# Optimization experiments

Hardware: AMD Instinct MI355X
Metric: run time of the kernel (lower is better)

Reference implementation:

```python
import jax, jax.numpy as jnp
import numpy as np

N = 50000  # num nodes
EPS = 1e-06


def setup_inputs() -> dict:
    key = jax.random.key(0)
    ks = jax.random.split(key, 7)
    E = 800000
    nfeat, nhid, nclass = 64, 128, 64
    x = jax.random.normal(ks[0], (N, nfeat), dtype=jnp.float32)
    src = jax.random.randint(ks[1], (E,), 0, N, dtype=jnp.int32)
    dst = jax.random.randint(ks[2], (E,), 0, N, dtype=jnp.int32)
    W1 = jax.random.normal(ks[3], (nfeat, nhid), dtype=jnp.float32) * (1.0 / np.sqrt(nfeat))
    b1 = jnp.zeros((nhid,), dtype=jnp.float32)
    W2 = jax.random.normal(ks[4], (nhid, nclass), dtype=jnp.float32) * (1.0 / np.sqrt(nhid))
    b2 = jnp.zeros((nclass,), dtype=jnp.float32)
    return {"x": x, "src": src, "dst": dst, "W1": W1, "b1": b1, "W2": W2, "b2": b2}


def _sage_conv(h, src, dst, W, b):
    # spmm(adj, h): sum of neighbor features per destination row
    num = jax.ops.segment_sum(h[src], dst, num_segments=N)  # [N, d]
    # spmm(adj, ones_like(h)): per-row degree broadcast over features
    deg = jax.ops.segment_sum(jnp.ones((src.shape[0],), dtype=h.dtype), dst, num_segments=N)
    neighbor_mean = num / (deg[:, None] + EPS)
    return neighbor_mean @ W + b


def reference(x, src, dst, W1, b1, W2, b2):
    h = jax.nn.relu(_sage_conv(x, src, dst, W1, b1))
    # dropout is identity in eval mode (training=False)
    h = _sage_conv(h, src, dst, W2, b2)
    return jax.nn.log_softmax(h, axis=1)
```

## Files before the change

kernel.cpp:

```cpp
#include <hip/hip_runtime.h>
#include <hip/hip_fp16.h>

#define N_NODES 50000
#define EPS 1e-6f
#define NPAD 50048
#define CAP 64

#define NBKT 512
#define NPB 98
#define NROWS (NBKT * NPB)
#define BCAP 2048
#define CHUNK_A 3072
#define XH8 (N_NODES * 64 / 8)


#define COMP(v, j) ((j) == 0 ? (v).x : (j) == 1 ? (v).y : (j) == 2 ? (v).z : (v).w)

__device__ __forceinline__ float4 h4_to_f4(uint2 u) {
  __half2 h0 = *reinterpret_cast<__half2*>(&u.x);
  __half2 h1 = *reinterpret_cast<__half2*>(&u.y);
  float2 f0 = __half22float2(h0);
  float2 f1 = __half22float2(h1);
  float4 r; r.x = f0.x; r.y = f0.y; r.z = f1.x; r.w = f1.y;
  return r;
}

__global__ __launch_bounds__(256) void bucketize_kernel(
    const int* __restrict__ src, const int* __restrict__ dst,
    int* __restrict__ bcur, int* __restrict__ packed,
    const float* __restrict__ x, __half* __restrict__ xh, int E) {
  __shared__ int lcnt[NBKT];
  __shared__ int lbase[NBKT];
  int t = threadIdx.x;

  for (int i = blockIdx.x * 256 + t; i < XH8; i += gridDim.x * 256) {
    float4 a = ((const float4*)x)[2 * i];
    float4 b = ((const float4*)x)[2 * i + 1];
    __half2 h0 = __floats2half2_rn(a.x, a.y);
    __half2 h1 = __floats2half2_rn(a.z, a.w);
    __half2 h2 = __floats2half2_rn(b.x, b.y);
    __half2 h3 = __floats2half2_rn(b.z, b.w);
    uint4 o;
    o.x = *(unsigned int*)&h0; o.y = *(unsigned int*)&h1;
    o.z = *(unsigned int*)&h2; o.w = *(unsigned int*)&h3;
    ((uint4*)xh)[i] = o;
  }

  lcnt[t] = 0; lcnt[t + 256] = 0;
  __syncthreads();
  int base = blockIdx.x * CHUNK_A;
  int end = base + CHUNK_A; if (end > E) end = E;
  for (int e = base + t; e < end; e += 256) atomicAdd(&lcnt[dst[e] / NPB], 1);
  __syncthreads();
  {
    int c0 = lcnt[t], c1 = lcnt[t + 256];
    lbase[t]       = c0 ? atomicAdd(&bcur[t], c0) : 0;
    lbase[t + 256] = c1 ? atomicAdd(&bcur[t + 256], c1) : 0;
    lcnt[t] = 0; lcnt[t + 256] = 0;
  }
  __syncthreads();
  for (int e = base + t; e < end; e += 256) {
    int d = dst[e];
    int b = d / NPB;
    int pos = lbase[b] + atomicAdd(&lcnt[b], 1);
    if (pos < BCAP)
      packed[(b << 11) + pos] = (src[e] << 8) | (d - b * NPB);
  }
}

__global__ __launch_bounds__(256) void rows_kernel(
    const int* __restrict__ bcur, const int* __restrict__ packed,
    int* __restrict__ cnt, int* __restrict__ ssrc) {
  __shared__ int lout[NPB * 64];
  __shared__ int lcnt[NPB];
  int t = threadIdx.x;
  int b = blockIdx.x;
  if (t < NPB) lcnt[t] = 0;
  __syncthreads();
  int count = bcur[b]; if (count > BCAP) count = BCAP;
  const int* pk = packed + (b << 11);
  for (int i = t; i < count; i += 256) {
    int p = pk[i];
    int dl = p & 0xff;
    int pos = atomicAdd(&lcnt[dl], 1);
    if (pos < CAP) lout[(dl << 6) + pos] = p >> 8;
  }
  __syncthreads();
  int4* d4 = (int4*)(ssrc + (size_t)b * (NPB * 64));
  const int4* s4 = (const int4*)lout;
  for (int i = t; i < NPB * 16; i += 256) d4[i] = s4[i];
  if (t < NPB) {
    int c = lcnt[t]; if (c > CAP) c = CAP;
    cnt[b * NPB + t] = c;
  }
}

#define QADD(V0, V1, V2, V3) do {                                         \
    acc.x += ((V0).x + (V1).x) + ((V2).x + (V3).x);                       \
    acc.y += ((V0).y + (V1).y) + ((V2).y + (V3).y);                       \
    acc.z += ((V0).z + (V1).z) + ((V2).z + (V3).z);                       \
    acc.w += ((V0).w + (V1).w) + ((V2).w + (V3).w);                       \
  } while (0)

#define ADD1(V) do {                                                      \
    acc.x += (V).x; acc.y += (V).y; acc.z += (V).z; acc.w += (V).w;       \
  } while (0)

#define GATHER_STEP_H(SRCPTR)                                             \
  {                                                                       \
    int rem = e - base; if (rem > 16) rem = 16;                           \
    int s[16];                                                            \
    _Pragma("unroll")                                                     \
    for (int j = 0; j < 16; j++) s[j] = ssrc[base + j];                   \
    _Pragma("unroll")                                                     \
    for (int j = 0; j < 16; j++) { if (j >= rem) s[j] = 0; }              \
    uint2 v[16];                                                          \
    _Pragma("unroll")                                                     \
    for (int j = 0; j < 16; j++)                                          \
      v[j] = ((const uint2*)((SRCPTR) + (size_t)s[j] * 64))[l16];         \
    int rq = rem >> 2, rr = rem & 3;                                      \
    _Pragma("unroll")                                                     \
    for (int q = 0; q < 4; q++) {                                         \
      if (q < rq) {                                                       \
        float4 f0 = h4_to_f4(v[4 * q]);                                   \
        float4 f1 = h4_to_f4(v[4 * q + 1]);                               \
        float4 f2 = h4_to_f4(v[4 * q + 2]);                               \
        float4 f3 = h4_to_f4(v[4 * q + 3]);                               \
        QADD(f0, f1, f2, f3);                                             \
      }                                                                   \
    }                                                                     \
    _Pragma("unroll")                                                     \
    for (int q = 0; q < 4; q++) {                                         \
      if (q == rq && rr > 0) {                                            \
        float4 f0 = h4_to_f4(v[4 * q]);                                   \
        ADD1(f0);                                                         \
        if (rr > 1) { float4 f1 = h4_to_f4(v[4 * q + 1]); ADD1(f1); }     \
        if (rr > 2) { float4 f2 = h4_to_f4(v[4 * q + 2]); ADD1(f2); }     \
      }                                                                   \
    }                                                                     \
  }

__global__ __launch_bounds__(256) void gather1_kernel(
    const __half* __restrict__ xh, const int* __restrict__ cnt,
    const int* __restrict__ ssrc, __half* __restrict__ mean1h) {
  int t = threadIdx.x;
  int lane = t & 63;
  int sub = lane >> 4;
  int l16 = lane & 15;
  int node = blockIdx.x * 16 + ((t >> 6) << 2) + sub;
  int b = node << 6;
  int e = b + cnt[node];
  float4 acc = {0.f, 0.f, 0.f, 0.f};
  for (int base = b; base < e; base += 16) {
    GATHER_STEP_H(xh)
  }
  float dinv = 1.0f / ((float)(e - b) + EPS);
  __half2 p0 = __floats2half2_rn(acc.x * dinv, acc.y * dinv);
  __half2 p1 = __floats2half2_rn(acc.z * dinv, acc.w * dinv);
  uint2 o;
  o.x = *(unsigned int*)&p0; o.y = *(unsigned int*)&p1;
  ((uint2*)(mean1h + (size_t)node * 64))[l16] = o;
}

__global__ __launch_bounds__(256, 3) void mlp_fused_kernel(
    const __half* __restrict__ mean1h, const float* __restrict__ W1,
    const float* __restrict__ b1, const float* __restrict__ W2,
    __half* __restrict__ gh) {
  __shared__ float sM[64][68];
  __shared__ float sH[64][132];
  int t = threadIdx.x;
  int row0 = blockIdx.x * 64;

  {
    const uint2* M2 = (const uint2*)(mean1h + (size_t)row0 * 64);
#pragma unroll
    for (int i = 0; i < 4; i++) {
      int idx = t + 256 * i;
      float4 f = h4_to_f4(M2[idx]);
      *(float4*)&sM[idx >> 4][(idx & 15) << 2] = f;
    }
  }
  __syncthreads();

  int tc = t & 15;
  int tr = t >> 4;

  {
    int c = tc << 3;
    int r = tr << 2;
    float acc[4][8];
    float4 bA = *(const float4*)(b1 + c);
    float4 bB = *(const float4*)(b1 + c + 4);
#pragma unroll
    for (int i = 0; i < 4; i++) {
      acc[i][0] = bA.x; acc[i][1] = bA.y; acc[i][2] = bA.z; acc[i][3] = bA.w;
      acc[i][4] = bB.x; acc[i][5] = bB.y; acc[i][6] = bB.z; acc[i][7] = bB.w;
    }
#pragma unroll 1
    for (int k = 0; k < 64; k += 4) {
      float4 a[4];
#pragma unroll
      for (int i = 0; i < 4; i++) a[i] = *(const float4*)&sM[r + i][k];
      float4 wA[4], wB[4];
#pragma unroll
      for (int j = 0; j < 4; j++) {
        const float* wrow = W1 + (size_t)(k + j) * 128 + c;
        wA[j] = *(const float4*)wrow;
        wB[j] = *(const float4*)(wrow + 4);
      }
#pragma unroll
      for (int j = 0; j < 4; j++) {
#pragma unroll
        for (int i = 0; i < 4; i++) {
          float av = COMP(a[i], j);
          acc[i][0] = fmaf(av, wA[j].x, acc[i][0]);
          acc[i][1] = fmaf(av, wA[j].y, acc[i][1]);
          acc[i][2] = fmaf(av, wA[j].z, acc[i][2]);
          acc[i][3] = fmaf(av, wA[j].w, acc[i][3]);
          acc[i][4] = fmaf(av, wB[j].x, acc[i][4]);
          acc[i][5] = fmaf(av, wB[j].y, acc[i][5]);
          acc[i][6] = fmaf(av, wB[j].z, acc[i][6]);
          acc[i][7] = fmaf(av, wB[j].w, acc[i][7]);
        }
      }
    }
#pragma unroll
    for (int i = 0; i < 4; i++) {
      float4 h0, h1v;
      h0.x = fmaxf(acc[i][0], 0.f); h0.y = fmaxf(acc[i][1], 0.f);
      h0.z = fmaxf(acc[i][2], 0.f); h0.w = fmaxf(acc[i][3], 0.f);
      h1v.x = fmaxf(acc[i][4], 0.f); h1v.y = fmaxf(acc[i][5], 0.f);
      h1v.z = fmaxf(acc[i][6], 0.f); h1v.w = fmaxf(acc[i][7], 0.f);
      *(float4*)&sH[r + i][c] = h0;
      *(float4*)&sH[r + i][c + 4] = h1v;
    }
  }
  __syncthreads();

  {
    int c = tc << 2;
    int r = tr << 2;
    float acc[4][4];
#pragma unroll
    for (int i = 0; i < 4; i++)
      acc[i][0] = acc[i][1] = acc[i][2] = acc[i][3] = 0.f;
#pragma unroll 1
    for (int k = 0; k < 128; k += 4) {
      float4 a[4];
#pragma unroll
      for (int i = 0; i < 4; i++) a[i] = *(const float4*)&sH[r + i][k];
      float4 w[4];
#pragma unroll
      for (int j = 0; j < 4; j++)
        w[j] = *(const float4*)(W2 + (size_t)(k + j) * 64 + c);
#pragma unroll
      for (int j = 0; j < 4; j++) {
#pragma unroll
        for (int i = 0; i < 4; i++) {
          float av = COMP(a[i], j);
          acc[i][0] = fmaf(av, w[j].x, acc[i][0]);
          acc[i][1] = fmaf(av, w[j].y, acc[i][1]);
          acc[i][2] = fmaf(av, w[j].z, acc[i][2]);
          acc[i][3] = fmaf(av, w[j].w, acc[i][3]);
        }
      }
    }
#pragma unroll
    for (int i = 0; i < 4; i++) {
      int row = row0 + r + i;
      if (row < N_NODES) {
        __half2 p0 = __floats2half2_rn(acc[i][0], acc[i][1]);
        __half2 p1 = __floats2half2_rn(acc[i][2], acc[i][3]);
        uint2 o;
        o.x = *(unsigned int*)&p0; o.y = *(unsigned int*)&p1;
        *(uint2*)(gh + (size_t)row * 64 + c) = o;
      }
    }
  }
}

__global__ __launch_bounds__(256) void gather2_kernel(
    const __half* __restrict__ gh, const int* __restrict__ cnt,
    const int* __restrict__ ssrc, const float* __restrict__ b2,
    float* __restrict__ out) {
  int t = threadIdx.x;
  int lane = t & 63;
  int sub = lane >> 4;
  int l16 = lane & 15;
  int node = blockIdx.x * 16 + ((t >> 6) << 2) + sub;
  int b = node << 6;
  int e = b + cnt[node];
  float4 acc = {0.f, 0.f, 0.f, 0.f};
  for (int base = b; base < e; base += 16) {
    GATHER_STEP_H(gh)
  }
  float dinv = 1.0f / ((float)(e - b) + EPS);
  float4 b2v = ((const float4*)b2)[l16];
  float4 val;
  val.x = acc.x * dinv + b2v.x;
  val.y = acc.y * dinv + b2v.y;
  val.z = acc.z * dinv + b2v.z;
  val.w = acc.w * dinv + b2v.w;

  float4 m = val;
#pragma unroll
  for (int o = 8; o > 0; o >>= 1) {
    m.x = fmaxf(m.x, __shfl_xor(m.x, o, 64));
    m.y = fmaxf(m.y, __shfl_xor(m.y, o, 64));
    m.z = fmaxf(m.z, __shfl_xor(m.z, o, 64));
    m.w = fmaxf(m.w, __shfl_xor(m.w, o, 64));
  }
  float mx = fmaxf(fmaxf(m.x, m.z), fmaxf(m.y, m.w));

  float4 ex;
  ex.x = __expf(val.x - mx);
  ex.y = __expf(val.y - mx);
  ex.z = __expf(val.z - mx);
  ex.w = __expf(val.w - mx);
#pragma unroll
  for (int o = 8; o > 0; o >>= 1) {
    ex.x += __shfl_xor(ex.x, o, 64);
    ex.y += __shfl_xor(ex.y, o, 64);
    ex.z += __shfl_xor(ex.z, o, 64);
    ex.w += __shfl_xor(ex.w, o, 64);
  }
  float sm = (ex.x + ex.z) + (ex.y + ex.w);

  float ls = logf(sm);
  float4 o4;
  o4.x = (val.x - mx) - ls;
  o4.y = (val.y - mx) - ls;
  o4.z = (val.z - mx) - ls;
  o4.w = (val.w - mx) - ls;
  ((float4*)(out + (size_t)node * 64))[l16] = o4;
}

extern "C" void kernel_launch(void* const* d_in, const int* in_sizes, int n_in,
                              void* d_out, int out_size, void* d_ws, size_t ws_size,
                              hipStream_t stream) {
  const float* x   = (const float*)d_in[0];
  const int*   src = (const int*)d_in[1];
  const int*   dst = (const int*)d_in[2];
  const float* W1  = (const float*)d_in[3];
  const float* b1  = (const float*)d_in[4];
  const float* W2  = (const float*)d_in[5];
  const float* b2  = (const float*)d_in[6];
  float* out = (float*)d_out;
  int E = in_sizes[1];

  int* bcur   = (int*)d_ws;
  int* packed = bcur + NBKT;
  int* cnt    = packed + (size_t)NBKT * BCAP;
  int* ssrc   = cnt + NROWS;
  __half* mean1h = (__half*)(ssrc + (size_t)NROWS * 64);
  __half* xh   = mean1h + (size_t)NPAD * 64;
  __half* gh   = xh + (size_t)NPAD * 64;

  hipMemsetAsync(bcur, 0, NBKT * sizeof(int), stream);
  bucketize_kernel<<<(E + CHUNK_A - 1) / CHUNK_A, 256, 0, stream>>>(
      src, dst, bcur, packed, x, xh, E);
  rows_kernel<<<NBKT, 256, 0, stream>>>(bcur, packed, cnt, ssrc);
  gather1_kernel<<<N_NODES / 16, 256, 0, stream>>>(xh, cnt, ssrc, mean1h);
  mlp_fused_kernel<<<NPAD / 64, 256, 0, stream>>>(mean1h, W1, b1, W2, gh);
  gather2_kernel<<<N_NODES / 16, 256, 0, stream>>>(gh, cnt, ssrc, b2, out);
}
```

Measured before the change: 173.7 us.

## Rewrite fused MLP with fp16 MFMA matrix instructions

Replaces the scalar FP32 FMA tiled GEMMs in the fused two-layer MLP with MFMA 16x16x32 fp16 instructions. Each block stages the mean features, plus transposed fp16 copies of W1 and W2, in shared memory. Results are written back through a shared staging tile so the stores to global memory are coalesced. This aims to cut the ALU cost of the MLP stage. In exchange it uses more LDS per block, repeats the weight transpose and conversion in every block, and rounds the weights to fp16.

```diff
diff --git a/kernel.cpp b/kernel.cpp
--- a/kernel.cpp
+++ b/kernel.cpp
@@ -15,6 +15,9 @@
 
 
 #define COMP(v, j) ((j) == 0 ? (v).x : (j) == 1 ? (v).y : (j) == 2 ? (v).z : (v).w)
+
+typedef _Float16 half8 __attribute__((ext_vector_type(8)));
+typedef float floatx4 __attribute__((ext_vector_type(4)));
 
 __device__ __forceinline__ float4 h4_to_f4(uint2 u) {
   __half2 h0 = *reinterpret_cast<__half2*>(&u.x);
@@ -162,120 +165,121 @@
   ((uint2*)(mean1h + (size_t)node * 64))[l16] = o;
 }
 
-__global__ __launch_bounds__(256, 3) void mlp_fused_kernel(
+__global__ __launch_bounds__(256) void mlp_mfma_kernel(
     const __half* __restrict__ mean1h, const float* __restrict__ W1,
     const float* __restrict__ b1, const float* __restrict__ W2,
     __half* __restrict__ gh) {
-  __shared__ float sM[64][68];
-  __shared__ float sH[64][132];
+  __shared__ __align__(16) char smem[62464];
+  __half (*sM)[72]    = (__half(*)[72])smem;
+  __half (*sW1T)[72]  = (__half(*)[72])(smem + 9216);
+  __half (*sH)[136]   = (__half(*)[136])(smem + 27648);
+  __half (*sW2T)[136] = (__half(*)[136])(smem + 45056);
+  __half (*sG)[64]    = (__half(*)[64])smem;
+
   int t = threadIdx.x;
   int row0 = blockIdx.x * 64;
 
   {
-    const uint2* M2 = (const uint2*)(mean1h + (size_t)row0 * 64);
-#pragma unroll
-    for (int i = 0; i < 4; i++) {
+    const uint4* M4 = (const uint4*)(mean1h + (size_t)row0 * 64);
+#pragma unroll
+    for (int i = 0; i < 2; i++) {
       int idx = t + 256 * i;
-      float4 f = h4_to_f4(M2[idx]);
-      *(float4*)&sM[idx >> 4][(idx & 15) << 2] = f;
+      uint4 v = M4[idx];
+      *(uint4*)&sM[idx >> 3][(idx & 7) * 8] = v;
     }
   }
-  __syncthreads();
-
-  int tc = t & 15;
-  int tr = t >> 4;
+#pragma unroll
+  for (int i = 0; i < 8; i++) {
+    int idx = t + 256 * i;
+    int k = idx >> 5, c4 = (idx & 31) * 4;
+    float4 w = *(const float4*)(W1 + (size_t)k * 128 + c4);
+    sW1T[c4 + 0][k] = __float2half(w.x);
+    sW1T[c4 + 1][k] = __float2half(w.y);
+    sW1T[c4 + 2][k] = __float2half(w.z);
+    sW1T[c4 + 3][k] = __float2half(w.w);
+  }
+#pragma unroll
+  for (int i = 0; i < 8; i++) {
+    int idx = t + 256 * i;
+    int k = idx >> 4, c4 = (idx & 15) * 4;
+    float4 w = *(const float4*)(W2 + (size_t)k * 64 + c4);
+    sW2T[c4 + 0][k] = __float2half(w.x);
+    sW2T[c4 + 1][k] = __float2half(w.y);
+    sW2T[c4 + 2][k] = __float2half(w.z);
+    sW2T[c4 + 3][k] = __float2half(w.w);
+  }
+  __syncthreads();
+
+  int l = t & 63, wv = t >> 6;
+  int l16 = l & 15, lg = l >> 4;
 
   {
-    int c = tc << 3;
-    int r = tr << 2;
-    float acc[4][8];
-    float4 bA = *(const float4*)(b1 + c);
-    float4 bB = *(const float4*)(b1 + c + 4);
-#pragma unroll
-    for (int i = 0; i < 4; i++) {
-      acc[i][0] = bA.x; acc[i][1] = bA.y; acc[i][2] = bA.z; acc[i][3] = bA.w;
-      acc[i][4] = bB.x; acc[i][5] = bB.y; acc[i][6] = bB.z; acc[i][7] = bB.w;
+    floatx4 acc[4][2];
+#pragma unroll
+    for (int tc = 0; tc < 2; tc++) {
+      float bias = b1[(2 * wv + tc) * 16 + l16];
+#pragma unroll
+      for (int tr = 0; tr < 4; tr++)
+        acc[tr][tc] = (floatx4){bias, bias, bias, bias};
     }
-#pragma unroll 1
-    for (int k = 0; k < 64; k += 4) {
-      float4 a[4];
-#pragma unroll
-      for (int i = 0; i < 4; i++) a[i] = *(const float4*)&sM[r + i][k];
-      float4 wA[4], wB[4];
-#pragma unroll
-      for (int j = 0; j < 4; j++) {
-        const float* wrow = W1 + (size_t)(k + j) * 128 + c;
-        wA[j] = *(const float4*)wrow;
-        wB[j] = *(const float4*)(wrow + 4);
-      }
-#pragma unroll
-      for (int j = 0; j < 4; j++) {
-#pragma unroll
-        for (int i = 0; i < 4; i++) {
-          float av = COMP(a[i], j);
-          acc[i][0] = fmaf(av, wA[j].x, acc[i][0]);
-          acc[i][1] = fmaf(av, wA[j].y, acc[i][1]);
-          acc[i][2] = fmaf(av, wA[j].z, acc[i][2]);
-          acc[i][3] = fmaf(av, wA[j].w, acc[i][3]);
-          acc[i][4] = fmaf(av, wB[j].x, acc[i][4]);
-          acc[i][5] = fmaf(av, wB[j].y, acc[i][5]);
-          acc[i][6] = fmaf(av, wB[j].z, acc[i][6]);
-          acc[i][7] = fmaf(av, wB[j].w, acc[i][7]);
+#pragma unroll
+    for (int kb = 0; kb < 2; kb++) {
+      half8 a[4], bf[2];
+#pragma unroll
+      for (int tr = 0; tr < 4; tr++)
+        a[tr] = *(const half8*)&sM[tr * 16 + l16][kb * 32 + lg * 8];
+#pragma unroll
+      for (int tc = 0; tc < 2; tc++)
+        bf[tc] = *(const half8*)&sW1T[(2 * wv + tc) * 16 + l16][kb * 32 + lg * 8];
+#pragma unroll
+      for (int tc = 0; tc < 2; tc++)
+#pragma unroll
+        for (int tr = 0; tr < 4; tr++)
+          acc[tr][tc] = __builtin_amdgcn_mfma_f32_16x16x32_f16(
+              a[tr], bf[tc], acc[tr][tc], 0, 0, 0);
+    }
+#pragma unroll
+    for (int tc = 0; tc < 2; tc++)
+#pragma unroll
+      for (int tr = 0; tr < 4; tr++)
+#pragma unroll
+        for (int r = 0; r < 4; r++) {
+          float h = fmaxf(acc[tr][tc][r], 0.f);
+          sH[tr * 16 + lg * 4 + r][(2 * wv + tc) * 16 + l16] = __float2half(h);
         }
+  }
+  __syncthreads();
+
+  {
+    floatx4 acc[4];
+#pragma unroll
+    for (int tc = 0; tc < 4; tc++) acc[tc] = (floatx4){0.f, 0.f, 0.f, 0.f};
+    half8 a[4];
+#pragma unroll
+    for (int kb = 0; kb < 4; kb++)
+      a[kb] = *(const half8*)&sH[wv * 16 + l16][kb * 32 + lg * 8];
+#pragma unroll
+    for (int tc = 0; tc < 4; tc++) {
+#pragma unroll
+      for (int kb = 0; kb < 4; kb++) {
+        half8 bf = *(const half8*)&sW2T[tc * 16 + l16][kb * 32 + lg * 8];
+        acc[tc] = __builtin_amdgcn_mfma_f32_16x16x32_f16(a[kb], bf, acc[tc], 0, 0, 0);
       }
     }
 #pragma unroll
-    for (int i = 0; i < 4; i++) {
-      float4 h0, h1v;
-      h0.x = fmaxf(acc[i][0], 0.f); h0.y = fmaxf(acc[i][1], 0.f);
-      h0.z = fmaxf(acc[i][2], 0.f); h0.w = fmaxf(acc[i][3], 0.f);
-      h1v.x = fmaxf(acc[i][4], 0.f); h1v.y = fmaxf(acc[i][5], 0.f);
-      h1v.z = fmaxf(acc[i][6], 0.f); h1v.w = fmaxf(acc[i][7], 0.f);
-      *(float4*)&sH[r + i][c] = h0;
-      *(float4*)&sH[r + i][c + 4] = h1v;
-    }
-  }
-  __syncthreads();
-
-  {
-    int c = tc << 2;
-    int r = tr << 2;
-    float acc[4][4];
-#pragma unroll
-    for (int i = 0; i < 4; i++)
-      acc[i][0] = acc[i][1] = acc[i][2] = acc[i][3] = 0.f;
-#pragma unroll 1
-    for (int k = 0; k < 128; k += 4) {
-      float4 a[4];
-#pragma unroll
-      for (int i = 0; i < 4; i++) a[i] = *(const float4*)&sH[r + i][k];
-      float4 w[4];
-#pragma unroll
-      for (int j = 0; j < 4; j++)
-        w[j] = *(const float4*)(W2 + (size_t)(k + j) * 64 + c);
-#pragma unroll
-      for (int j = 0; j < 4; j++) {
-#pragma unroll
-        for (int i = 0; i < 4; i++) {
-          float av = COMP(a[i], j);
-          acc[i][0] = fmaf(av, w[j].x, acc[i][0]);
-          acc[i][1] = fmaf(av, w[j].y, acc[i][1]);
-          acc[i][2] = fmaf(av, w[j].z, acc[i][2]);
-          acc[i][3] = fmaf(av, w[j].w, acc[i][3]);
-        }
-      }
-    }
-#pragma unroll
-    for (int i = 0; i < 4; i++) {
-      int row = row0 + r + i;
-      if (row < N_NODES) {
-        __half2 p0 = __floats2half2_rn(acc[i][0], acc[i][1]);
-        __half2 p1 = __floats2half2_rn(acc[i][2], acc[i][3]);
-        uint2 o;
-        o.x = *(unsigned int*)&p0; o.y = *(unsigned int*)&p1;
-        *(uint2*)(gh + (size_t)row * 64 + c) = o;
-      }
-    }
+    for (int tc = 0; tc < 4; tc++)
+#pragma unroll
+      for (int r = 0; r < 4; r++)
+        sG[wv * 16 + lg * 4 + r][tc * 16 + l16] = __float2half(acc[tc][r]);
+  }
+  __syncthreads();
+
+#pragma unroll
+  for (int i = 0; i < 4; i++) {
+    int idx = t + 256 * i;
+    int row = idx >> 4, c4 = (idx & 15) * 4;
+    if (row0 + row < N_NODES)
+      *(uint2*)(gh + (size_t)(row0 + row) * 64 + c4) = *(uint2*)&sG[row][c4];
   }
 }
 
@@ -361,6 +365,6 @@
       src, dst, bcur, packed, x, xh, E);
   rows_kernel<<<NBKT, 256, 0, stream>>>(bcur, packed, cnt, ssrc);
   gather1_kernel<<<N_NODES / 16, 256, 0, stream>>>(xh, cnt, ssrc, mean1h);
-  mlp_fused_kernel<<<NPAD / 64, 256, 0, stream>>>(mean1h, W1, b1, W2, gh);
+  mlp_mfma_kernel<<<NPAD / 64, 256, 0, stream>>>(mean1h, W1, b1, W2, gh);
   gather2_kernel<<<N_NODES / 16, 256, 0, stream>>>(gh, cnt, ssrc, b2, out);
 }
```

After: 159.9 us. 7.9% less time.
